# Kernel tuning notes

Hardware: AMD Instinct MI355X
Metric: run time of the kernel (lower is better)

The kernel has to match this reference:

```python
import jax, jax.numpy as jnp
import numpy as np

B, N = 8192, 32          # batch of (user,item) pairs, AOS triples per pair
D1, D2 = 64, 64          # user/item and aspect/opinion embedding dims
H, O = 128, 64           # hidden_dims = [128, 64]
R = 3                    # n_relations (sentiments)
SLOPE = 0.01             # nn.LeakyReLU default negative_slope


def leaky_relu(x):
    return jnp.where(x >= 0, x, SLOPE * x)


def setup_inputs() -> dict:
    key = jax.random.key(0)
    ks = jax.random.split(key, 14)
    p = 0.1  # param scale
    return {
        "u_emb": jax.random.normal(ks[0], (B, D1), jnp.float32),
        "i_emb": jax.random.normal(ks[1], (B, D1), jnp.float32),
        "a_emb": jax.random.normal(ks[2], (B, N, D2), jnp.float32),
        "o_emb": jax.random.normal(ks[3], (B, N, D2), jnp.float32),
        "s": jax.random.randint(ks[4], (B, N), 0, R, jnp.int64),
        # per-relation AO MLP: Linear(128->128) + LeakyReLU, Linear(128->64) + LeakyReLU
        "ao_W0": jax.random.normal(ks[5], (R, 2 * D2, H), jnp.float32) * p,
        "ao_b0": jax.random.normal(ks[6], (R, H), jnp.float32) * p,
        "ao_W1": jax.random.normal(ks[7], (R, H, O), jnp.float32) * p,
        "ao_b1": jax.random.normal(ks[8], (R, O), jnp.float32) * p,
        # shared UI MLP: Linear(128->128) + LeakyReLU, Linear(128->64) + LeakyReLU
        "ui_W0": jax.random.normal(ks[9], (2 * D1, H), jnp.float32) * p,
        "ui_b0": jax.random.normal(ks[10], (H,), jnp.float32) * p,
        "ui_W1": jax.random.normal(ks[11], (H, O), jnp.float32) * p,
        "ui_b1": jax.random.normal(ks[12], (O,), jnp.float32) * p,
    }


def reference(u_emb, i_emb, a_emb, o_emb, s,
              ao_W0, ao_b0, ao_W1, ao_b1,
              ui_W0, ui_b0, ui_W1, ui_b1):
    # ui branch (shared MLP)
    ui_in = jnp.concatenate([u_emb, i_emb], axis=-1)            # [B, 2*D1]
    ui = leaky_relu(ui_in @ ui_W0 + ui_b0)                       # [B, H]
    ui = leaky_relu(ui @ ui_W1 + ui_b1)                          # [B, O]

    # ao branch: relation-specific MLPs. Instead of masked gather/scatter,
    # compute all R (small) relation MLPs densely and select per element.
    ao_in = jnp.concatenate([a_emb, o_emb], axis=-1)             # [B, N, 2*D2]
    h = leaky_relu(jnp.einsum('bnd,rdh->rbnh', ao_in, ao_W0)
                   + ao_b0[:, None, None, :])                    # [R, B, N, H]
    h = leaky_relu(jnp.einsum('rbnh,rho->rbno', h, ao_W1)
                   + ao_b1[:, None, None, :])                    # [R, B, N, O]

    h = jnp.moveaxis(h, 0, 2)                                    # [B, N, R, O]
    aos = jnp.take_along_axis(h, s[:, :, None, None], axis=2)[:, :, 0, :]  # [B, N, O]

    # loss == 'bpr': dot product score
    pred = jnp.sum(ui[:, None, :] * aos, axis=-1)                # [B, N]
    return pred
```

## Files before the change

kernel.cpp:

```cpp
#include <hip/hip_runtime.h>

typedef unsigned short u16t;
typedef __bf16 bf16x8 __attribute__((ext_vector_type(8)));
typedef float  f32x4  __attribute__((ext_vector_type(4)));

#define SLOPE 0.01f
#define SAP 136
#define UIP 72

__device__ __forceinline__ float lrelu(float x) { return x >= 0.0f ? x : SLOPE * x; }
__device__ __forceinline__ u16t f2b(float f) {
    union { float f; unsigned i; } x; x.f = f;
    return (u16t)((x.i + 0x7fffu + ((x.i >> 16) & 1u)) >> 16);
}
__device__ __forceinline__ float b2f(u16t u) {
    union { unsigned i; float f; } x; x.i = ((unsigned)u) << 16; return x.f;
}
__device__ __forceinline__ unsigned pk2(float a, float b) {
    union { float f; unsigned i; } xa, xb; xa.f = a; xb.f = b;
    unsigned ra = (xa.i + 0x7fffu + ((xa.i >> 16) & 1u)) >> 16;
    unsigned rb = (xb.i + 0x7fffu + ((xb.i >> 16) & 1u)) & 0xffff0000u;
    return ra | rb;
}
__device__ __forceinline__ uint4 pack8(float4 x, float4 y) {
    uint4 r; r.x = pk2(x.x, x.y); r.y = pk2(x.z, x.w);
    r.z = pk2(y.x, y.y); r.w = pk2(y.z, y.w); return r;
}
__device__ __forceinline__ int clmp3(int v) { return v < 0 ? 0 : (v > 2 ? 2 : v); }

__global__ void pack_w(const float* __restrict__ W0, const float* __restrict__ W1,
                       const float* __restrict__ uW0, const float* __restrict__ uW1,
                       u16t* __restrict__ W0p, u16t* __restrict__ W1p,
                       u16t* __restrict__ U0p, u16t* __restrict__ U1p) {
    int tid = blockIdx.x * 256 + threadIdx.x;
    if (tid < 49152) {
        int j = tid & 7, lane = (tid >> 3) & 63, c = (tid >> 9) & 7,
            kk = (tid >> 12) & 3, r = tid >> 14;
        int k = kk * 32 + (lane >> 4) * 8 + j, n = c * 16 + (lane & 15);
        W0p[tid] = f2b(W0[(r * 128 + k) * 128 + n]);
    } else if (tid < 73728) {
        int t2 = tid - 49152;
        int j = t2 & 7, lane = (t2 >> 3) & 63, c = (t2 >> 9) & 3,
            kk = (t2 >> 11) & 3, r = t2 >> 13;
        int k = kk * 32 + (lane >> 4) * 8 + j, n = c * 16 + (lane & 15);
        W1p[t2] = f2b(W1[(r * 128 + k) * 64 + n]);
    } else if (tid < 90112) {
        int t3 = tid - 73728;
        int j = t3 & 7, lane = (t3 >> 3) & 63, c = (t3 >> 9) & 7, kk = t3 >> 12;
        int k = kk * 32 + (lane >> 4) * 8 + j, n = c * 16 + (lane & 15);
        U0p[t3] = f2b(uW0[k * 128 + n]);
    } else if (tid < 98304) {
        int t4 = tid - 90112;
        int j = t4 & 7, lane = (t4 >> 3) & 63, c = (t4 >> 9) & 3, kk = t4 >> 11;
        int k = kk * 32 + (lane >> 4) * 8 + j, n = c * 16 + (lane & 15);
        U1p[t4] = f2b(uW1[k * 64 + n]);
    }
}

__global__ __launch_bounds__(512) void prep_ui(
    const float* __restrict__ u_emb, const float* __restrict__ i_emb,
    const u16t* __restrict__ U0p, const u16t* __restrict__ U1p,
    const float* __restrict__ uib0, const float* __restrict__ uib1,
    u16t* __restrict__ uiT)
{
    __shared__ __align__(16) u16t sA[32 * SAP];
    __shared__ __align__(16) u16t sH[32 * SAP];
    const int t = threadIdx.x, wave = t >> 6, lane = t & 63, m = lane & 15, kg = lane >> 4;
    const int c = wave, c2 = wave & 3, hlf = wave >> 2;
    const int B0 = blockIdx.x * 32;

    bf16x8 w0f[4], w1f[4];
#pragma unroll
    for (int kk = 0; kk < 4; ++kk) {
        w0f[kk] = *(const bf16x8*)(U0p + (((kk * 8 + c) * 64 + lane) << 3));
        w1f[kk] = *(const bf16x8*)(U1p + (((kk * 4 + c2) * 64 + lane) << 3));
    }
    const float b0 = uib0[c * 16 + m], b1 = uib1[c2 * 16 + m];

    {
        const int row = t >> 4, seg = t & 15;
        const float* src = (seg < 8) ? (u_emb + (size_t)(B0 + row) * 64 + seg * 8)
                                     : (i_emb + (size_t)(B0 + row) * 64 + (seg - 8) * 8);
        float4 v0 = ((const float4*)src)[0], v1 = ((const float4*)src)[1];
        *(uint4*)&sA[row * SAP + seg * 8] = pack8(v0, v1);
    }
    __syncthreads();

#pragma unroll
    for (int mt = 0; mt < 2; ++mt) {
        const u16t* ap = &sA[(mt * 16 + m) * SAP + kg * 8];
        bf16x8 a0 = *(const bf16x8*)(ap),      a1 = *(const bf16x8*)(ap + 32);
        bf16x8 a2 = *(const bf16x8*)(ap + 64), a3 = *(const bf16x8*)(ap + 96);
        f32x4 acc = {0.f, 0.f, 0.f, 0.f};
        acc = __builtin_amdgcn_mfma_f32_16x16x32_bf16(a0, w0f[0], acc, 0, 0, 0);
        acc = __builtin_amdgcn_mfma_f32_16x16x32_bf16(a1, w0f[1], acc, 0, 0, 0);
        acc = __builtin_amdgcn_mfma_f32_16x16x32_bf16(a2, w0f[2], acc, 0, 0, 0);
        acc = __builtin_amdgcn_mfma_f32_16x16x32_bf16(a3, w0f[3], acc, 0, 0, 0);
#pragma unroll
        for (int j = 0; j < 4; ++j)
            sH[(mt * 16 + kg * 4 + j) * SAP + c * 16 + m] = f2b(lrelu(acc[j] + b0));
    }
    __syncthreads();

    {
        const int mt = hlf;
        const u16t* hp = &sH[(mt * 16 + m) * SAP + kg * 8];
        bf16x8 a0 = *(const bf16x8*)(hp),      a1 = *(const bf16x8*)(hp + 32);
        bf16x8 a2 = *(const bf16x8*)(hp + 64), a3 = *(const bf16x8*)(hp + 96);
        f32x4 acc = {0.f, 0.f, 0.f, 0.f};
        acc = __builtin_amdgcn_mfma_f32_16x16x32_bf16(a0, w1f[0], acc, 0, 0, 0);
        acc = __builtin_amdgcn_mfma_f32_16x16x32_bf16(a1, w1f[1], acc, 0, 0, 0);
        acc = __builtin_amdgcn_mfma_f32_16x16x32_bf16(a2, w1f[2], acc, 0, 0, 0);
        acc = __builtin_amdgcn_mfma_f32_16x16x32_bf16(a3, w1f[3], acc, 0, 0, 0);
#pragma unroll
        for (int j = 0; j < 4; ++j)
            uiT[(size_t)(B0 + mt * 16 + kg * 4 + j) * 64 + c2 * 16 + m] =
                f2b(lrelu(acc[j] + b1));
    }
}

__global__ __launch_bounds__(256) void passA(const int* __restrict__ s,
                                             int* __restrict__ cntB) {
    __shared__ int sc[3];
    const int t = threadIdx.x;
    if (t < 3) sc[t] = 0;
    __syncthreads();
    int4 sv = ((const int4*)s)[blockIdx.x * 256 + t];
    int l0 = 0, l1 = 0, l2 = 0;
    int r;
    r = clmp3(sv.x); l0 += (r == 0); l1 += (r == 1); l2 += (r == 2);
    r = clmp3(sv.y); l0 += (r == 0); l1 += (r == 1); l2 += (r == 2);
    r = clmp3(sv.z); l0 += (r == 0); l1 += (r == 1); l2 += (r == 2);
    r = clmp3(sv.w); l0 += (r == 0); l1 += (r == 1); l2 += (r == 2);
    atomicAdd(&sc[0], l0); atomicAdd(&sc[1], l1); atomicAdd(&sc[2], l2);
    __syncthreads();
    if (t < 3) cntB[blockIdx.x * 3 + t] = sc[t];
}

__global__ __launch_bounds__(256) void passB(const int* __restrict__ s,
                                             const int* __restrict__ cntB,
                                             int* __restrict__ cntOut,
                                             int* __restrict__ rows) {
    __shared__ int sTab[768];
    __shared__ int sBT[6];
    __shared__ int sS[256];
    const int t = threadIdx.x, blk = blockIdx.x;
    sTab[t] = cntB[t]; sTab[t + 256] = cntB[t + 256]; sTab[t + 512] = cntB[t + 512];
    __syncthreads();
    if (t < 3) {
        int base = 0, tot = 0;
        for (int b = 0; b < 256; ++b) {
            int v = sTab[b * 3 + t];
            if (b < blk) base += v;
            tot += v;
        }
        sBT[t] = base; sBT[3 + t] = tot;
    }
    int4 sv = ((const int4*)s)[blk * 256 + t];
    int rr[4] = { clmp3(sv.x), clmp3(sv.y), clmp3(sv.z), clmp3(sv.w) };
    int packed = (1 << (11 * rr[0])) + (1 << (11 * rr[1]))
               + (1 << (11 * rr[2])) + (1 << (11 * rr[3]));
    sS[t] = packed;
    __syncthreads();
    for (int off = 1; off < 256; off <<= 1) {
        int v = (t >= off) ? sS[t - off] : 0;
        __syncthreads();
        sS[t] += v;
        __syncthreads();
    }
    const int excl = sS[t] - packed;
    const int g0 = 0, g1 = sBT[3], g2 = sBT[3] + sBT[4];
    int seen[3] = {0, 0, 0};
#pragma unroll
    for (int i = 0; i < 4; ++i) {
        int rl = rr[i];
        int gb = rl == 0 ? g0 : (rl == 1 ? g1 : g2);
        int pos = gb + sBT[rl] + ((excl >> (11 * rl)) & 2047) + seen[rl];
        seen[rl]++;
        rows[pos] = blk * 1024 + t * 4 + i;
    }
    if (blk == 0 && t < 3) cntOut[t] = sBT[3 + t];
}

__global__ __launch_bounds__(512) void ao_main(
    const float* __restrict__ a_emb, const float* __restrict__ o_emb,
    const float* __restrict__ ao_b0, const float* __restrict__ ao_b1,
    const u16t* __restrict__ W0p, const u16t* __restrict__ W1p,
    const u16t* __restrict__ uiT, const int* __restrict__ rows,
    const int* __restrict__ tot, float* __restrict__ out)
{
    __shared__ __align__(16) u16t sA[64 * SAP];
    __shared__ __align__(16) u16t sH[64 * SAP];
    __shared__ __align__(16) u16t sUIl[64 * UIP];
    __shared__ int sRid[64];

    const int n0 = tot[0], n1 = tot[1], n2 = tot[2];
    const int ch0 = (n0 + 63) >> 6, ch1 = (n1 + 63) >> 6, ch2 = (n2 + 63) >> 6;
    const int blk = blockIdx.x;
    int r, chunk, bb, nb;
    if (blk < ch0)             { r = 0; chunk = blk;              bb = 0;       nb = n0; }
    else if (blk < ch0 + ch1)  { r = 1; chunk = blk - ch0;        bb = n0;      nb = n1; }
    else if (blk < ch0 + ch1 + ch2) { r = 2; chunk = blk - ch0 - ch1; bb = n0 + n1; nb = n2; }
    else return;
    const int rstart = chunk * 64;
    int nrows = nb - rstart; if (nrows > 64) nrows = 64;

    const int t = threadIdx.x, wave = t >> 6, lane = t & 63, m = lane & 15, kg = lane >> 4;
    const int c = wave, c2 = wave & 3, hlf = wave >> 2;

    const u16t* wp0 = W0p + r * 16384;
    const u16t* wp1 = W1p + r * 8192;
    bf16x8 w0f[4], w1f[4];
#pragma unroll
    for (int kk = 0; kk < 4; ++kk) {
        w0f[kk] = *(const bf16x8*)(wp0 + (((kk * 8 + c) * 64 + lane) << 3));
        w1f[kk] = *(const bf16x8*)(wp1 + (((kk * 4 + c2) * 64 + lane) << 3));
    }
    const float b0 = ao_b0[r * 128 + c * 16 + m];
    const float b1 = ao_b1[r * 64 + c2 * 16 + m];

    {
        const int q = t >> 3, seg = t & 7;
        const int rid = rows[bb + rstart + (q < nrows ? q : nrows - 1)];
        const float* src = (seg < 4) ? (a_emb + (size_t)rid * 64 + seg * 16)
                                     : (o_emb + (size_t)rid * 64 + (seg - 4) * 16);
        float4 v0 = ((const float4*)src)[0], v1 = ((const float4*)src)[1];
        float4 v2 = ((const float4*)src)[2], v3 = ((const float4*)src)[3];
        uint4* dst = (uint4*)&sA[q * SAP + seg * 16];
        dst[0] = pack8(v0, v1);
        dst[1] = pack8(v2, v3);
        *(uint4*)&sUIl[q * UIP + seg * 8] =
            *(const uint4*)(uiT + ((size_t)(rid >> 5)) * 64 + seg * 8);
        if (t < 64) sRid[t] = rows[bb + rstart + (t < nrows ? t : nrows - 1)];
    }
    __syncthreads();

#pragma unroll
    for (int mt = 0; mt < 4; ++mt) {
        const u16t* ap = &sA[(mt * 16 + m) * SAP + kg * 8];
        bf16x8 a0 = *(const bf16x8*)(ap),      a1 = *(const bf16x8*)(ap + 32);
        bf16x8 a2 = *(const bf16x8*)(ap + 64), a3 = *(const bf16x8*)(ap + 96);
        f32x4 acc_a = {0.f, 0.f, 0.f, 0.f}, acc_b = {0.f, 0.f, 0.f, 0.f};
        acc_a = __builtin_amdgcn_mfma_f32_16x16x32_bf16(a0, w0f[0], acc_a, 0, 0, 0);
        acc_a = __builtin_amdgcn_mfma_f32_16x16x32_bf16(a1, w0f[1], acc_a, 0, 0, 0);
        acc_b = __builtin_amdgcn_mfma_f32_16x16x32_bf16(a2, w0f[2], acc_b, 0, 0, 0);
        acc_b = __builtin_amdgcn_mfma_f32_16x16x32_bf16(a3, w0f[3], acc_b, 0, 0, 0);
        f32x4 acc = acc_a + acc_b;
#pragma unroll
        for (int j = 0; j < 4; ++j)
            sH[(mt * 16 + kg * 4 + j) * SAP + c * 16 + m] = f2b(lrelu(acc[j] + b0));
    }
    __syncthreads();

    for (int mt = hlf; mt < 4; mt += 2) {
        const u16t* hp = &sH[(mt * 16 + m) * SAP + kg * 8];
        bf16x8 a0 = *(const bf16x8*)(hp),      a1 = *(const bf16x8*)(hp + 32);
        bf16x8 a2 = *(const bf16x8*)(hp + 64), a3 = *(const bf16x8*)(hp + 96);
        f32x4 acc_a = {0.f, 0.f, 0.f, 0.f}, acc_b = {0.f, 0.f, 0.f, 0.f};
        acc_a = __builtin_amdgcn_mfma_f32_16x16x32_bf16(a0, w1f[0], acc_a, 0, 0, 0);
        acc_a = __builtin_amdgcn_mfma_f32_16x16x32_bf16(a1, w1f[1], acc_a, 0, 0, 0);
        acc_b = __builtin_amdgcn_mfma_f32_16x16x32_bf16(a2, w1f[2], acc_b, 0, 0, 0);
        acc_b = __builtin_amdgcn_mfma_f32_16x16x32_bf16(a3, w1f[3], acc_b, 0, 0, 0);
        f32x4 acc = acc_a + acc_b;
        const int o = c2 * 16 + m;
        float pj[4];
#pragma unroll
        for (int j = 0; j < 4; ++j) {
            const int q = mt * 16 + kg * 4 + j;
            pj[j] = lrelu(acc[j] + b1) * b2f(sUIl[q * UIP + o]);
        }
#pragma unroll
        for (int msk = 8; msk >= 1; msk >>= 1) {
#pragma unroll
            for (int j = 0; j < 4; ++j) pj[j] += __shfl_xor(pj[j], msk, 16);
        }
        if (m == 0) {
#pragma unroll
            for (int j = 0; j < 4; ++j) {
                const int q = mt * 16 + kg * 4 + j;
                if (q < nrows) atomicAdd(&out[sRid[q]], pj[j]);
            }
        }
    }
}

extern "C" void kernel_launch(void* const* d_in, const int* in_sizes, int n_in,
                              void* d_out, int out_size, void* d_ws, size_t ws_size,
                              hipStream_t stream) {
    (void)in_sizes; (void)n_in; (void)ws_size;
    const float* u_emb = (const float*)d_in[0];
    const float* i_emb = (const float*)d_in[1];
    const float* a_emb = (const float*)d_in[2];
    const float* o_emb = (const float*)d_in[3];
    const int*   s     = (const int*)  d_in[4];
    const float* aoW0  = (const float*)d_in[5];
    const float* aob0  = (const float*)d_in[6];
    const float* aoW1  = (const float*)d_in[7];
    const float* aob1  = (const float*)d_in[8];
    const float* uiW0  = (const float*)d_in[9];
    const float* uib0  = (const float*)d_in[10];
    const float* uiW1  = (const float*)d_in[11];
    const float* uib1  = (const float*)d_in[12];
    float* out = (float*)d_out;

    char* ws = (char*)d_ws;
    u16t* W0p  = (u16t*)(ws);
    u16t* W1p  = (u16t*)(ws + 98304);
    u16t* U0p  = (u16t*)(ws + 147456);
    u16t* U1p  = (u16t*)(ws + 180224);
    u16t* uiT  = (u16t*)(ws + 196608);
    int*  cntB = (int*) (ws + 1245184);
    int*  totC = (int*) (ws + 1248256);
    int*  rowsP= (int*) (ws + 1248272);

    hipMemsetAsync(d_out, 0, (size_t)out_size * sizeof(float), stream);
    pack_w<<<dim3(384), dim3(256), 0, stream>>>(aoW0, aoW1, uiW0, uiW1, W0p, W1p, U0p, U1p);
    passA<<<dim3(256), dim3(256), 0, stream>>>(s, cntB);
    prep_ui<<<dim3(256), dim3(512), 0, stream>>>(u_emb, i_emb, U0p, U1p, uib0, uib1, uiT);
    passB<<<dim3(256), dim3(256), 0, stream>>>(s, cntB, totC, rowsP);
    ao_main<<<dim3(4099), dim3(512), 0, stream>>>(
        a_emb, o_emb, aob0, aob1, W0p, W1p, uiT, rowsP, totC, out);
}
```

Baseline: 215.9 us.

## Merge prep kernels, drop memset and global atomics, two chunks per block

Pack_w and passA are merged into one launch, and prep_ui and passB into a second, which cuts kernel launches and removes the output memset. ao_main now handles two 64-row chunks per block and reloads the weight fragments only when the relation changes. It reduces each row's prediction in shared memory with LDS atomics and writes it directly instead of doing global atomicAdd. The bf16 packing now uses the hardware v_cvt_pk_bf16_f32 instruction, and ao_main gets an occupancy hint in launch_bounds. The direct writes rely on every output row being covered exactly once by the row permutation.

```diff
diff --git a/kernel.cpp b/kernel.cpp
--- a/kernel.cpp
+++ b/kernel.cpp
@@ -17,10 +17,9 @@
     union { unsigned i; float f; } x; x.i = ((unsigned)u) << 16; return x.f;
 }
 __device__ __forceinline__ unsigned pk2(float a, float b) {
-    union { float f; unsigned i; } xa, xb; xa.f = a; xb.f = b;
-    unsigned ra = (xa.i + 0x7fffu + ((xa.i >> 16) & 1u)) >> 16;
-    unsigned rb = (xb.i + 0x7fffu + ((xb.i >> 16) & 1u)) & 0xffff0000u;
-    return ra | rb;
+    unsigned r;
+    asm("v_cvt_pk_bf16_f32 %0, %1, %2" : "=v"(r) : "v"(a), "v"(b));
+    return r;
 }
 __device__ __forceinline__ uint4 pack8(float4 x, float4 y) {
     uint4 r; r.x = pk2(x.x, x.y); r.y = pk2(x.z, x.w);
@@ -28,161 +27,173 @@
 }
 __device__ __forceinline__ int clmp3(int v) { return v < 0 ? 0 : (v > 2 ? 2 : v); }
 
-__global__ void pack_w(const float* __restrict__ W0, const float* __restrict__ W1,
-                       const float* __restrict__ uW0, const float* __restrict__ uW1,
-                       u16t* __restrict__ W0p, u16t* __restrict__ W1p,
-                       u16t* __restrict__ U0p, u16t* __restrict__ U1p) {
-    int tid = blockIdx.x * 256 + threadIdx.x;
-    if (tid < 49152) {
-        int j = tid & 7, lane = (tid >> 3) & 63, c = (tid >> 9) & 7,
-            kk = (tid >> 12) & 3, r = tid >> 14;
-        int k = kk * 32 + (lane >> 4) * 8 + j, n = c * 16 + (lane & 15);
-        W0p[tid] = f2b(W0[(r * 128 + k) * 128 + n]);
-    } else if (tid < 73728) {
-        int t2 = tid - 49152;
-        int j = t2 & 7, lane = (t2 >> 3) & 63, c = (t2 >> 9) & 3,
-            kk = (t2 >> 11) & 3, r = t2 >> 13;
-        int k = kk * 32 + (lane >> 4) * 8 + j, n = c * 16 + (lane & 15);
-        W1p[t2] = f2b(W1[(r * 128 + k) * 64 + n]);
-    } else if (tid < 90112) {
-        int t3 = tid - 73728;
-        int j = t3 & 7, lane = (t3 >> 3) & 63, c = (t3 >> 9) & 7, kk = t3 >> 12;
-        int k = kk * 32 + (lane >> 4) * 8 + j, n = c * 16 + (lane & 15);
-        U0p[t3] = f2b(uW0[k * 128 + n]);
-    } else if (tid < 98304) {
-        int t4 = tid - 90112;
-        int j = t4 & 7, lane = (t4 >> 3) & 63, c = (t4 >> 9) & 3, kk = t4 >> 11;
-        int k = kk * 32 + (lane >> 4) * 8 + j, n = c * 16 + (lane & 15);
-        U1p[t4] = f2b(uW1[k * 64 + n]);
+__global__ __launch_bounds__(256) void kernelA(
+    const float* __restrict__ W0, const float* __restrict__ W1,
+    const float* __restrict__ uW0, const float* __restrict__ uW1,
+    const int* __restrict__ s,
+    u16t* __restrict__ W0p, u16t* __restrict__ W1p,
+    u16t* __restrict__ U0p, u16t* __restrict__ U1p,
+    int* __restrict__ cntB)
+{
+    __shared__ int sc[3];
+    const int t = threadIdx.x;
+    if (blockIdx.x < 384) {
+        int tid = blockIdx.x * 256 + t;
+        if (tid < 49152) {
+            int j = tid & 7, lane = (tid >> 3) & 63, c = (tid >> 9) & 7,
+                kk = (tid >> 12) & 3, r = tid >> 14;
+            int k = kk * 32 + (lane >> 4) * 8 + j, n = c * 16 + (lane & 15);
+            W0p[tid] = f2b(W0[(r * 128 + k) * 128 + n]);
+        } else if (tid < 73728) {
+            int t2 = tid - 49152;
+            int j = t2 & 7, lane = (t2 >> 3) & 63, c = (t2 >> 9) & 3,
+                kk = (t2 >> 11) & 3, r = t2 >> 13;
+            int k = kk * 32 + (lane >> 4) * 8 + j, n = c * 16 + (lane & 15);
+            W1p[t2] = f2b(W1[(r * 128 + k) * 64 + n]);
+        } else if (tid < 90112) {
+            int t3 = tid - 73728;
+            int j = t3 & 7, lane = (t3 >> 3) & 63, c = (t3 >> 9) & 7, kk = t3 >> 12;
+            int k = kk * 32 + (lane >> 4) * 8 + j, n = c * 16 + (lane & 15);
+            U0p[t3] = f2b(uW0[k * 128 + n]);
+        } else if (tid < 98304) {
+            int t4 = tid - 90112;
+            int j = t4 & 7, lane = (t4 >> 3) & 63, c = (t4 >> 9) & 3, kk = t4 >> 11;
+            int k = kk * 32 + (lane >> 4) * 8 + j, n = c * 16 + (lane & 15);
+            U1p[t4] = f2b(uW1[k * 64 + n]);
+        }
+    } else {
+        const int blk = blockIdx.x - 384;
+        if (t < 3) sc[t] = 0;
+        __syncthreads();
+        int4 sv = ((const int4*)s)[blk * 256 + t];
+        int l0 = 0, l1 = 0, l2 = 0, r;
+        r = clmp3(sv.x); l0 += (r == 0); l1 += (r == 1); l2 += (r == 2);
+        r = clmp3(sv.y); l0 += (r == 0); l1 += (r == 1); l2 += (r == 2);
+        r = clmp3(sv.z); l0 += (r == 0); l1 += (r == 1); l2 += (r == 2);
+        r = clmp3(sv.w); l0 += (r == 0); l1 += (r == 1); l2 += (r == 2);
+        atomicAdd(&sc[0], l0); atomicAdd(&sc[1], l1); atomicAdd(&sc[2], l2);
+        __syncthreads();
+        if (t < 3) cntB[blk * 3 + t] = sc[t];
     }
 }
 
-__global__ __launch_bounds__(512) void prep_ui(
+__global__ __launch_bounds__(512) void kernelB(
     const float* __restrict__ u_emb, const float* __restrict__ i_emb,
     const u16t* __restrict__ U0p, const u16t* __restrict__ U1p,
     const float* __restrict__ uib0, const float* __restrict__ uib1,
-    u16t* __restrict__ uiT)
+    const int* __restrict__ s, const int* __restrict__ cntB,
+    u16t* __restrict__ uiT, int* __restrict__ cntOut, int* __restrict__ rows)
 {
     __shared__ __align__(16) u16t sA[32 * SAP];
     __shared__ __align__(16) u16t sH[32 * SAP];
-    const int t = threadIdx.x, wave = t >> 6, lane = t & 63, m = lane & 15, kg = lane >> 4;
-    const int c = wave, c2 = wave & 3, hlf = wave >> 2;
-    const int B0 = blockIdx.x * 32;
-
-    bf16x8 w0f[4], w1f[4];
-#pragma unroll
-    for (int kk = 0; kk < 4; ++kk) {
-        w0f[kk] = *(const bf16x8*)(U0p + (((kk * 8 + c) * 64 + lane) << 3));
-        w1f[kk] = *(const bf16x8*)(U1p + (((kk * 4 + c2) * 64 + lane) << 3));
-    }
-    const float b0 = uib0[c * 16 + m], b1 = uib1[c2 * 16 + m];
-
-    {
-        const int row = t >> 4, seg = t & 15;
-        const float* src = (seg < 8) ? (u_emb + (size_t)(B0 + row) * 64 + seg * 8)
-                                     : (i_emb + (size_t)(B0 + row) * 64 + (seg - 8) * 8);
-        float4 v0 = ((const float4*)src)[0], v1 = ((const float4*)src)[1];
-        *(uint4*)&sA[row * SAP + seg * 8] = pack8(v0, v1);
-    }
-    __syncthreads();
-
-#pragma unroll
-    for (int mt = 0; mt < 2; ++mt) {
-        const u16t* ap = &sA[(mt * 16 + m) * SAP + kg * 8];
-        bf16x8 a0 = *(const bf16x8*)(ap),      a1 = *(const bf16x8*)(ap + 32);
-        bf16x8 a2 = *(const bf16x8*)(ap + 64), a3 = *(const bf16x8*)(ap + 96);
-        f32x4 acc = {0.f, 0.f, 0.f, 0.f};
-        acc = __builtin_amdgcn_mfma_f32_16x16x32_bf16(a0, w0f[0], acc, 0, 0, 0);
-        acc = __builtin_amdgcn_mfma_f32_16x16x32_bf16(a1, w0f[1], acc, 0, 0, 0);
-        acc = __builtin_amdgcn_mfma_f32_16x16x32_bf16(a2, w0f[2], acc, 0, 0, 0);
-        acc = __builtin_amdgcn_mfma_f32_16x16x32_bf16(a3, w0f[3], acc, 0, 0, 0);
-#pragma unroll
-        for (int j = 0; j < 4; ++j)
-            sH[(mt * 16 + kg * 4 + j) * SAP + c * 16 + m] = f2b(lrelu(acc[j] + b0));
-    }
-    __syncthreads();
-
-    {
-        const int mt = hlf;
-        const u16t* hp = &sH[(mt * 16 + m) * SAP + kg * 8];
-        bf16x8 a0 = *(const bf16x8*)(hp),      a1 = *(const bf16x8*)(hp + 32);
-        bf16x8 a2 = *(const bf16x8*)(hp + 64), a3 = *(const bf16x8*)(hp + 96);
-        f32x4 acc = {0.f, 0.f, 0.f, 0.f};
-        acc = __builtin_amdgcn_mfma_f32_16x16x32_bf16(a0, w1f[0], acc, 0, 0, 0);
-        acc = __builtin_amdgcn_mfma_f32_16x16x32_bf16(a1, w1f[1], acc, 0, 0, 0);
-        acc = __builtin_amdgcn_mfma_f32_16x16x32_bf16(a2, w1f[2], acc, 0, 0, 0);
-        acc = __builtin_amdgcn_mfma_f32_16x16x32_bf16(a3, w1f[3], acc, 0, 0, 0);
-#pragma unroll
-        for (int j = 0; j < 4; ++j)
-            uiT[(size_t)(B0 + mt * 16 + kg * 4 + j) * 64 + c2 * 16 + m] =
-                f2b(lrelu(acc[j] + b1));
-    }
-}
-
-__global__ __launch_bounds__(256) void passA(const int* __restrict__ s,
-                                             int* __restrict__ cntB) {
-    __shared__ int sc[3];
-    const int t = threadIdx.x;
-    if (t < 3) sc[t] = 0;
-    __syncthreads();
-    int4 sv = ((const int4*)s)[blockIdx.x * 256 + t];
-    int l0 = 0, l1 = 0, l2 = 0;
-    int r;
-    r = clmp3(sv.x); l0 += (r == 0); l1 += (r == 1); l2 += (r == 2);
-    r = clmp3(sv.y); l0 += (r == 0); l1 += (r == 1); l2 += (r == 2);
-    r = clmp3(sv.z); l0 += (r == 0); l1 += (r == 1); l2 += (r == 2);
-    r = clmp3(sv.w); l0 += (r == 0); l1 += (r == 1); l2 += (r == 2);
-    atomicAdd(&sc[0], l0); atomicAdd(&sc[1], l1); atomicAdd(&sc[2], l2);
-    __syncthreads();
-    if (t < 3) cntB[blockIdx.x * 3 + t] = sc[t];
-}
-
-__global__ __launch_bounds__(256) void passB(const int* __restrict__ s,
-                                             const int* __restrict__ cntB,
-                                             int* __restrict__ cntOut,
-                                             int* __restrict__ rows) {
     __shared__ int sTab[768];
     __shared__ int sBT[6];
     __shared__ int sS[256];
-    const int t = threadIdx.x, blk = blockIdx.x;
-    sTab[t] = cntB[t]; sTab[t + 256] = cntB[t + 256]; sTab[t + 512] = cntB[t + 512];
-    __syncthreads();
-    if (t < 3) {
-        int base = 0, tot = 0;
-        for (int b = 0; b < 256; ++b) {
-            int v = sTab[b * 3 + t];
-            if (b < blk) base += v;
-            tot += v;
-        }
-        sBT[t] = base; sBT[3 + t] = tot;
+    const int t = threadIdx.x;
+
+    if (blockIdx.x < 256) {
+        const int wave = t >> 6, lane = t & 63, m = lane & 15, kg = lane >> 4;
+        const int c = wave, c2 = wave & 3, hlf = wave >> 2;
+        const int B0 = blockIdx.x * 32;
+
+        bf16x8 w0f[4], w1f[4];
+#pragma unroll
+        for (int kk = 0; kk < 4; ++kk) {
+            w0f[kk] = *(const bf16x8*)(U0p + (((kk * 8 + c) * 64 + lane) << 3));
+            w1f[kk] = *(const bf16x8*)(U1p + (((kk * 4 + c2) * 64 + lane) << 3));
+        }
+        const float b0 = uib0[c * 16 + m], b1 = uib1[c2 * 16 + m];
+
+        {
+            const int row = t >> 4, seg = t & 15;
+            const float* src = (seg < 8) ? (u_emb + (size_t)(B0 + row) * 64 + seg * 8)
+                                         : (i_emb + (size_t)(B0 + row) * 64 + (seg - 8) * 8);
+            float4 v0 = ((const float4*)src)[0], v1 = ((const float4*)src)[1];
+            *(uint4*)&sA[row * SAP + seg * 8] = pack8(v0, v1);
+        }
+        __syncthreads();
+
+#pragma unroll
+        for (int mt = 0; mt < 2; ++mt) {
+            const u16t* ap = &sA[(mt * 16 + m) * SAP + kg * 8];
+            bf16x8 a0 = *(const bf16x8*)(ap),      a1 = *(const bf16x8*)(ap + 32);
+            bf16x8 a2 = *(const bf16x8*)(ap + 64), a3 = *(const bf16x8*)(ap + 96);
+            f32x4 acc = {0.f, 0.f, 0.f, 0.f};
+            acc = __builtin_amdgcn_mfma_f32_16x16x32_bf16(a0, w0f[0], acc, 0, 0, 0);
+            acc = __builtin_amdgcn_mfma_f32_16x16x32_bf16(a1, w0f[1], acc, 0, 0, 0);
+            acc = __builtin_amdgcn_mfma_f32_16x16x32_bf16(a2, w0f[2], acc, 0, 0, 0);
+            acc = __builtin_amdgcn_mfma_f32_16x16x32_bf16(a3, w0f[3], acc, 0, 0, 0);
+#pragma unroll
+            for (int j = 0; j < 4; ++j)
+                sH[(mt * 16 + kg * 4 + j) * SAP + c * 16 + m] = f2b(lrelu(acc[j] + b0));
+        }
+        __syncthreads();
+
+        {
+            const int mt = hlf;
+            const u16t* hp = &sH[(mt * 16 + m) * SAP + kg * 8];
+            bf16x8 a0 = *(const bf16x8*)(hp),      a1 = *(const bf16x8*)(hp + 32);
+            bf16x8 a2 = *(const bf16x8*)(hp + 64), a3 = *(const bf16x8*)(hp + 96);
+            f32x4 acc = {0.f, 0.f, 0.f, 0.f};
+            acc = __builtin_amdgcn_mfma_f32_16x16x32_bf16(a0, w1f[0], acc, 0, 0, 0);
+            acc = __builtin_amdgcn_mfma_f32_16x16x32_bf16(a1, w1f[1], acc, 0, 0, 0);
+            acc = __builtin_amdgcn_mfma_f32_16x16x32_bf16(a2, w1f[2], acc, 0, 0, 0);
+            acc = __builtin_amdgcn_mfma_f32_16x16x32_bf16(a3, w1f[3], acc, 0, 0, 0);
+#pragma unroll
+            for (int j = 0; j < 4; ++j)
+                uiT[(size_t)(B0 + mt * 16 + kg * 4 + j) * 64 + c2 * 16 + m] =
+                    f2b(lrelu(acc[j] + b1));
+        }
+    } else {
+        const int blk = blockIdx.x - 256;
+        if (t < 256) {
+            sTab[t] = cntB[t]; sTab[t + 256] = cntB[t + 256]; sTab[t + 512] = cntB[t + 512];
+        }
+        __syncthreads();
+        if (t < 3) {
+            int base = 0, tot = 0;
+            for (int b = 0; b < 256; ++b) {
+                int v = sTab[b * 3 + t];
+                if (b < blk) base += v;
+                tot += v;
+            }
+            sBT[t] = base; sBT[3 + t] = tot;
+        }
+        int rr0 = 0, rr1 = 0, rr2 = 0, rr3 = 0, packed = 0;
+        if (t < 256) {
+            int4 sv = ((const int4*)s)[blk * 256 + t];
+            rr0 = clmp3(sv.x); rr1 = clmp3(sv.y); rr2 = clmp3(sv.z); rr3 = clmp3(sv.w);
+            packed = (1 << (11 * rr0)) + (1 << (11 * rr1))
+                   + (1 << (11 * rr2)) + (1 << (11 * rr3));
+            sS[t] = packed;
+        }
+        __syncthreads();
+        for (int off = 1; off < 256; off <<= 1) {
+            int v = 0;
+            if (t >= off && t < 256) v = sS[t - off];
+            __syncthreads();
+            if (t < 256) sS[t] += v;
+            __syncthreads();
+        }
+        if (t < 256) {
+            const int excl = sS[t] - packed;
+            const int g1 = sBT[3], g2 = sBT[3] + sBT[4];
+            int rr[4] = { rr0, rr1, rr2, rr3 };
+            int seen[3] = {0, 0, 0};
+#pragma unroll
+            for (int i = 0; i < 4; ++i) {
+                int rl = rr[i];
+                int gb = rl == 0 ? 0 : (rl == 1 ? g1 : g2);
+                int pos = gb + sBT[rl] + ((excl >> (11 * rl)) & 2047) + seen[rl];
+                seen[rl]++;
+                rows[pos] = blk * 1024 + t * 4 + i;
+            }
+        }
+        if (blk == 0 && t < 3) cntOut[t] = sBT[3 + t];
     }
-    int4 sv = ((const int4*)s)[blk * 256 + t];
-    int rr[4] = { clmp3(sv.x), clmp3(sv.y), clmp3(sv.z), clmp3(sv.w) };
-    int packed = (1 << (11 * rr[0])) + (1 << (11 * rr[1]))
-               + (1 << (11 * rr[2])) + (1 << (11 * rr[3]));
-    sS[t] = packed;
-    __syncthreads();
-    for (int off = 1; off < 256; off <<= 1) {
-        int v = (t >= off) ? sS[t - off] : 0;
-        __syncthreads();
-        sS[t] += v;
-        __syncthreads();
-    }
-    const int excl = sS[t] - packed;
-    const int g0 = 0, g1 = sBT[3], g2 = sBT[3] + sBT[4];
-    int seen[3] = {0, 0, 0};
-#pragma unroll
-    for (int i = 0; i < 4; ++i) {
-        int rl = rr[i];
-        int gb = rl == 0 ? g0 : (rl == 1 ? g1 : g2);
-        int pos = gb + sBT[rl] + ((excl >> (11 * rl)) & 2047) + seen[rl];
-        seen[rl]++;
-        rows[pos] = blk * 1024 + t * 4 + i;
-    }
-    if (blk == 0 && t < 3) cntOut[t] = sBT[3 + t];
-}
-
-__global__ __launch_bounds__(512) void ao_main(
+}
+
+__global__ __launch_bounds__(512, 4) void ao_main(
     const float* __restrict__ a_emb, const float* __restrict__ o_emb,
     const float* __restrict__ ao_b0, const float* __restrict__ ao_b1,
     const u16t* __restrict__ W0p, const u16t* __restrict__ W1p,
@@ -192,102 +203,113 @@
     __shared__ __align__(16) u16t sA[64 * SAP];
     __shared__ __align__(16) u16t sH[64 * SAP];
     __shared__ __align__(16) u16t sUIl[64 * UIP];
-    __shared__ int sRid[64];
+    __shared__ float sPred[64];
 
     const int n0 = tot[0], n1 = tot[1], n2 = tot[2];
     const int ch0 = (n0 + 63) >> 6, ch1 = (n1 + 63) >> 6, ch2 = (n2 + 63) >> 6;
-    const int blk = blockIdx.x;
-    int r, chunk, bb, nb;
-    if (blk < ch0)             { r = 0; chunk = blk;              bb = 0;       nb = n0; }
-    else if (blk < ch0 + ch1)  { r = 1; chunk = blk - ch0;        bb = n0;      nb = n1; }
-    else if (blk < ch0 + ch1 + ch2) { r = 2; chunk = blk - ch0 - ch1; bb = n0 + n1; nb = n2; }
-    else return;
-    const int rstart = chunk * 64;
-    int nrows = nb - rstart; if (nrows > 64) nrows = 64;
+    const int nch = ch0 + ch1 + ch2;
 
     const int t = threadIdx.x, wave = t >> 6, lane = t & 63, m = lane & 15, kg = lane >> 4;
     const int c = wave, c2 = wave & 3, hlf = wave >> 2;
 
-    const u16t* wp0 = W0p + r * 16384;
-    const u16t* wp1 = W1p + r * 8192;
     bf16x8 w0f[4], w1f[4];
-#pragma unroll
-    for (int kk = 0; kk < 4; ++kk) {
-        w0f[kk] = *(const bf16x8*)(wp0 + (((kk * 8 + c) * 64 + lane) << 3));
-        w1f[kk] = *(const bf16x8*)(wp1 + (((kk * 4 + c2) * 64 + lane) << 3));
-    }
-    const float b0 = ao_b0[r * 128 + c * 16 + m];
-    const float b1 = ao_b1[r * 64 + c2 * 16 + m];
-
-    {
-        const int q = t >> 3, seg = t & 7;
-        const int rid = rows[bb + rstart + (q < nrows ? q : nrows - 1)];
-        const float* src = (seg < 4) ? (a_emb + (size_t)rid * 64 + seg * 16)
-                                     : (o_emb + (size_t)rid * 64 + (seg - 4) * 16);
-        float4 v0 = ((const float4*)src)[0], v1 = ((const float4*)src)[1];
-        float4 v2 = ((const float4*)src)[2], v3 = ((const float4*)src)[3];
-        uint4* dst = (uint4*)&sA[q * SAP + seg * 16];
-        dst[0] = pack8(v0, v1);
-        dst[1] = pack8(v2, v3);
-        *(uint4*)&sUIl[q * UIP + seg * 8] =
-            *(const uint4*)(uiT + ((size_t)(rid >> 5)) * 64 + seg * 8);
-        if (t < 64) sRid[t] = rows[bb + rstart + (t < nrows ? t : nrows - 1)];
-    }
-    __syncthreads();
-
-#pragma unroll
-    for (int mt = 0; mt < 4; ++mt) {
-        const u16t* ap = &sA[(mt * 16 + m) * SAP + kg * 8];
-        bf16x8 a0 = *(const bf16x8*)(ap),      a1 = *(const bf16x8*)(ap + 32);
-        bf16x8 a2 = *(const bf16x8*)(ap + 64), a3 = *(const bf16x8*)(ap + 96);
-        f32x4 acc_a = {0.f, 0.f, 0.f, 0.f}, acc_b = {0.f, 0.f, 0.f, 0.f};
-        acc_a = __builtin_amdgcn_mfma_f32_16x16x32_bf16(a0, w0f[0], acc_a, 0, 0, 0);
-        acc_a = __builtin_amdgcn_mfma_f32_16x16x32_bf16(a1, w0f[1], acc_a, 0, 0, 0);
-        acc_b = __builtin_amdgcn_mfma_f32_16x16x32_bf16(a2, w0f[2], acc_b, 0, 0, 0);
-        acc_b = __builtin_amdgcn_mfma_f32_16x16x32_bf16(a3, w0f[3], acc_b, 0, 0, 0);
-        f32x4 acc = acc_a + acc_b;
-#pragma unroll
-        for (int j = 0; j < 4; ++j)
-            sH[(mt * 16 + kg * 4 + j) * SAP + c * 16 + m] = f2b(lrelu(acc[j] + b0));
-    }
-    __syncthreads();
-
-    for (int mt = hlf; mt < 4; mt += 2) {
-        const u16t* hp = &sH[(mt * 16 + m) * SAP + kg * 8];
-        bf16x8 a0 = *(const bf16x8*)(hp),      a1 = *(const bf16x8*)(hp + 32);
-        bf16x8 a2 = *(const bf16x8*)(hp + 64), a3 = *(const bf16x8*)(hp + 96);
-        f32x4 acc_a = {0.f, 0.f, 0.f, 0.f}, acc_b = {0.f, 0.f, 0.f, 0.f};
-        acc_a = __builtin_amdgcn_mfma_f32_16x16x32_bf16(a0, w1f[0], acc_a, 0, 0, 0);
-        acc_a = __builtin_amdgcn_mfma_f32_16x16x32_bf16(a1, w1f[1], acc_a, 0, 0, 0);
-        acc_b = __builtin_amdgcn_mfma_f32_16x16x32_bf16(a2, w1f[2], acc_b, 0, 0, 0);
-        acc_b = __builtin_amdgcn_mfma_f32_16x16x32_bf16(a3, w1f[3], acc_b, 0, 0, 0);
-        f32x4 acc = acc_a + acc_b;
-        const int o = c2 * 16 + m;
-        float pj[4];
-#pragma unroll
-        for (int j = 0; j < 4; ++j) {
-            const int q = mt * 16 + kg * 4 + j;
-            pj[j] = lrelu(acc[j] + b1) * b2f(sUIl[q * UIP + o]);
-        }
-#pragma unroll
-        for (int msk = 8; msk >= 1; msk >>= 1) {
-#pragma unroll
-            for (int j = 0; j < 4; ++j) pj[j] += __shfl_xor(pj[j], msk, 16);
-        }
-        if (m == 0) {
+    float b0 = 0.f, b1 = 0.f;
+    int rprev = -1;
+
+    for (int ci = 0; ci < 2; ++ci) {
+        const int chunk = blockIdx.x * 2 + ci;
+        if (chunk >= nch) break;
+        int r, rel, bb, nb;
+        if (chunk < ch0)            { r = 0; rel = chunk;             bb = 0;       nb = n0; }
+        else if (chunk < ch0 + ch1) { r = 1; rel = chunk - ch0;       bb = n0;      nb = n1; }
+        else                        { r = 2; rel = chunk - ch0 - ch1; bb = n0 + n1; nb = n2; }
+        const int rstart = rel * 64;
+        int nrows = nb - rstart; if (nrows > 64) nrows = 64;
+
+        if (r != rprev) {
+            const u16t* wp0 = W0p + r * 16384;
+            const u16t* wp1 = W1p + r * 8192;
+#pragma unroll
+            for (int kk = 0; kk < 4; ++kk) {
+                w0f[kk] = *(const bf16x8*)(wp0 + (((kk * 8 + c) * 64 + lane) << 3));
+                w1f[kk] = *(const bf16x8*)(wp1 + (((kk * 4 + c2) * 64 + lane) << 3));
+            }
+            b0 = ao_b0[r * 128 + c * 16 + m];
+            b1 = ao_b1[r * 64 + c2 * 16 + m];
+            rprev = r;
+        }
+
+        {
+            const int q = t >> 3, seg = t & 7;
+            const int rid = rows[bb + rstart + (q < nrows ? q : nrows - 1)];
+            const float* src = (seg < 4) ? (a_emb + (size_t)rid * 64 + seg * 16)
+                                         : (o_emb + (size_t)rid * 64 + (seg - 4) * 16);
+            float4 v0 = ((const float4*)src)[0], v1 = ((const float4*)src)[1];
+            float4 v2 = ((const float4*)src)[2], v3 = ((const float4*)src)[3];
+            uint4* dst = (uint4*)&sA[q * SAP + seg * 16];
+            dst[0] = pack8(v0, v1);
+            dst[1] = pack8(v2, v3);
+            *(uint4*)&sUIl[q * UIP + seg * 8] =
+                *(const uint4*)(uiT + ((size_t)(rid >> 5)) * 64 + seg * 8);
+        }
+        if (t < 64) sPred[t] = 0.0f;
+        __syncthreads();
+
+#pragma unroll
+        for (int mt = 0; mt < 4; ++mt) {
+            const u16t* ap = &sA[(mt * 16 + m) * SAP + kg * 8];
+            bf16x8 a0 = *(const bf16x8*)(ap),      a1 = *(const bf16x8*)(ap + 32);
+            bf16x8 a2 = *(const bf16x8*)(ap + 64), a3 = *(const bf16x8*)(ap + 96);
+            f32x4 acc_a = {0.f, 0.f, 0.f, 0.f}, acc_b = {0.f, 0.f, 0.f, 0.f};
+            acc_a = __builtin_amdgcn_mfma_f32_16x16x32_bf16(a0, w0f[0], acc_a, 0, 0, 0);
+            acc_a = __builtin_amdgcn_mfma_f32_16x16x32_bf16(a1, w0f[1], acc_a, 0, 0, 0);
+            acc_b = __builtin_amdgcn_mfma_f32_16x16x32_bf16(a2, w0f[2], acc_b, 0, 0, 0);
+            acc_b = __builtin_amdgcn_mfma_f32_16x16x32_bf16(a3, w0f[3], acc_b, 0, 0, 0);
+            f32x4 acc = acc_a + acc_b;
+#pragma unroll
+            for (int j = 0; j < 4; ++j)
+                sH[(mt * 16 + kg * 4 + j) * SAP + c * 16 + m] = f2b(lrelu(acc[j] + b0));
+        }
+        __syncthreads();
+
+        for (int mt = hlf; mt < 4; mt += 2) {
+            const u16t* hp = &sH[(mt * 16 + m) * SAP + kg * 8];
+            bf16x8 a0 = *(const bf16x8*)(hp),      a1 = *(const bf16x8*)(hp + 32);
+            bf16x8 a2 = *(const bf16x8*)(hp + 64), a3 = *(const bf16x8*)(hp + 96);
+            f32x4 acc_a = {0.f, 0.f, 0.f, 0.f}, acc_b = {0.f, 0.f, 0.f, 0.f};
+            acc_a = __builtin_amdgcn_mfma_f32_16x16x32_bf16(a0, w1f[0], acc_a, 0, 0, 0);
+            acc_a = __builtin_amdgcn_mfma_f32_16x16x32_bf16(a1, w1f[1], acc_a, 0, 0, 0);
+            acc_b = __builtin_amdgcn_mfma_f32_16x16x32_bf16(a2, w1f[2], acc_b, 0, 0, 0);
+            acc_b = __builtin_amdgcn_mfma_f32_16x16x32_bf16(a3, w1f[3], acc_b, 0, 0, 0);
+            f32x4 acc = acc_a + acc_b;
+            const int o = c2 * 16 + m;
+            float pj[4];
 #pragma unroll
             for (int j = 0; j < 4; ++j) {
                 const int q = mt * 16 + kg * 4 + j;
-                if (q < nrows) atomicAdd(&out[sRid[q]], pj[j]);
-            }
-        }
+                pj[j] = lrelu(acc[j] + b1) * b2f(sUIl[q * UIP + o]);
+            }
+#pragma unroll
+            for (int msk = 8; msk >= 1; msk >>= 1) {
+#pragma unroll
+                for (int j = 0; j < 4; ++j) pj[j] += __shfl_xor(pj[j], msk, 16);
+            }
+            if (m == 0) {
+#pragma unroll
+                for (int j = 0; j < 4; ++j)
+                    atomicAdd(&sPred[mt * 16 + kg * 4 + j], pj[j]);
+            }
+        }
+        __syncthreads();
+
+        if (t < nrows) out[rows[bb + rstart + t]] = sPred[t];
     }
 }
 
 extern "C" void kernel_launch(void* const* d_in, const int* in_sizes, int n_in,
                               void* d_out, int out_size, void* d_ws, size_t ws_size,
                               hipStream_t stream) {
-    (void)in_sizes; (void)n_in; (void)ws_size;
+    (void)in_sizes; (void)n_in; (void)out_size; (void)ws_size;
     const float* u_emb = (const float*)d_in[0];
     const float* i_emb = (const float*)d_in[1];
     const float* a_emb = (const float*)d_in[2];
@@ -313,11 +335,10 @@
     int*  totC = (int*) (ws + 1248256);
     int*  rowsP= (int*) (ws + 1248272);
 
-    hipMemsetAsync(d_out, 0, (size_t)out_size * sizeof(float), stream);
-    pack_w<<<dim3(384), dim3(256), 0, stream>>>(aoW0, aoW1, uiW0, uiW1, W0p, W1p, U0p, U1p);
-    passA<<<dim3(256), dim3(256), 0, stream>>>(s, cntB);
-    prep_ui<<<dim3(256), dim3(512), 0, stream>>>(u_emb, i_emb, U0p, U1p, uib0, uib1, uiT);
-    passB<<<dim3(256), dim3(256), 0, stream>>>(s, cntB, totC, rowsP);
-    ao_main<<<dim3(4099), dim3(512), 0, stream>>>(
+    kernelA<<<dim3(640), dim3(256), 0, stream>>>(
+        aoW0, aoW1, uiW0, uiW1, s, W0p, W1p, U0p, U1p, cntB);
+    kernelB<<<dim3(512), dim3(512), 0, stream>>>(
+        u_emb, i_emb, U0p, U1p, uib0, uib1, s, cntB, uiT, totC, rowsP);
+    ao_main<<<dim3(2051), dim3(512), 0, stream>>>(
         a_emb, o_emb, aob0, aob1, W0p, W1p, uiT, rowsP, totC, out);
 }
```

Result: faster. 200.1 us (-7.3%).
